# Kernel tuning notes

Hardware: AMD Instinct MI355X
Metric: run time of the kernel (lower is better)

## Reference

```python
import jax, jax.numpy as jnp
import numpy as np

K = 32
BN_EPS = 1e-5


def setup_inputs() -> dict:
    key = jax.random.key(0)
    ks = jax.random.split(key, 4)
    B, Cin, N, C = 8, 1152, 4096, 128
    return {
        "x": jax.random.normal(ks[0], (B, Cin, N), dtype=jnp.float32),
        "W1": jax.random.normal(ks[1], (C, Cin), dtype=jnp.float32) * 0.02,
        "bn_gamma": jnp.ones((C,), jnp.float32),
        "bn_beta": jnp.zeros((C,), jnp.float32),
        "bn_mean": jnp.zeros((C,), jnp.float32),
        "bn_var": jnp.ones((C,), jnp.float32),
        "Wq": jax.random.normal(ks[2], (C, C), dtype=jnp.float32) * 0.05,
        "Wk": jax.random.normal(ks[3], (C, C), dtype=jnp.float32) * 0.05,
    }


def _forward(x, W1, bn_gamma, bn_beta, bn_mean, bn_var, Wq, Wk):
    # conv1: 1x1 Conv1d (no bias) + BatchNorm (inference stats) + LeakyReLU(0.2)
    h = jnp.einsum('oc,bcn->bon', W1, x)                       # [B,128,N]
    h = (h - bn_mean[None, :, None]) * jax.lax.rsqrt(bn_var + BN_EPS)[None, :, None]
    h = h * bn_gamma[None, :, None] + bn_beta[None, :, None]
    h = jnp.where(h >= 0, h, 0.2 * h)
    f = jnp.transpose(h, (0, 2, 1))                            # [B,N,128]

    # ops.group: feature-space KNN + 'diff' grouping
    sq = jnp.sum(f * f, axis=-1)                               # [B,N]
    dist = sq[:, :, None] + sq[:, None, :] - 2.0 * jnp.einsum('bnc,bmc->bnm', f, f)
    _, idx = jax.lax.top_k(-dist, K)                           # [B,N,K]
    nb = jax.vmap(lambda fb, ib: fb[ib])(f, idx)               # [B,N,K,128]
    diff = nb - f[:, :, None, :]                               # neighbors - center

    # q/k 1x1 convs, per-point 1xK attention
    q = jnp.einsum('bnc,oc->bno', f, Wq)                       # [B,N,128]
    k = jnp.einsum('bnkc,oc->bnko', diff, Wk)                  # [B,N,K,128]
    energy = jnp.einsum('bnc,bnkc->bnk', q, k) / jnp.sqrt(jnp.float32(q.shape[-1]))
    attn = jax.nn.softmax(energy, axis=-1)                     # [B,N,K]

    # std over K (biased), then per-cloud standardize (unbiased std, torch default)
    s = jnp.std(attn, axis=-1)                                 # [B,N]
    mean = jnp.mean(s, axis=1, keepdims=True)
    std = jnp.std(s, axis=1, keepdims=True, ddof=1)
    z = (s - mean) / std
    return 1.0 / (1.0 + jnp.power(jnp.float32(20.0), -z))      # modified sigmoid


def reference(x, W1, bn_gamma, bn_beta, bn_mean, bn_var, Wq, Wk):
    return _forward(x, W1, bn_gamma, bn_beta, bn_mean, bn_var, Wq, Wk)
```

## Files before the change

### kernel.cpp

```cpp
#include <hip/hip_runtime.h>
#include <math.h>

#define B_   8
#define CIN  1152
#define NPTS 4096
#define CH   128
#define KNN  32

__global__ __launch_bounds__(256) void k_conv_bn(
    const float* __restrict__ x, const float* __restrict__ W1,
    const float* __restrict__ gamma, const float* __restrict__ beta,
    const float* __restrict__ bmean, const float* __restrict__ bvar,
    float* __restrict__ f)
{
  __shared__ float Wl[8][132];
  __shared__ float Xl[8][36];
  int bid = blockIdx.x;
  int b = bid & 7;
  int nbase = (bid >> 3) * 32;
  int t = threadIdx.x;
  int c0 = (t & 31) * 4, n0 = (t >> 5) * 4;
  double acc[4][4];
#pragma unroll
  for (int i = 0; i < 4; ++i)
#pragma unroll
    for (int j = 0; j < 4; ++j) acc[i][j] = 0.0;

  for (int k0 = 0; k0 < CIN; k0 += 8) {
    {
      int c = t >> 1, kp = (t & 1) * 4;
      float4 w4 = *(const float4*)&W1[(size_t)c * CIN + k0 + kp];
      Wl[kp + 0][c] = w4.x; Wl[kp + 1][c] = w4.y;
      Wl[kp + 2][c] = w4.z; Wl[kp + 3][c] = w4.w;
    }
    {
      int k = t >> 5, n = t & 31;
      Xl[k][n] = x[((size_t)b * CIN + (k0 + k)) * NPTS + nbase + n];
    }
    __syncthreads();
#pragma unroll
    for (int kk = 0; kk < 8; ++kk) {
      float4 a  = *(const float4*)&Wl[kk][c0];
      float4 b0 = *(const float4*)&Xl[kk][n0];
      double av[4] = {(double)a.x, (double)a.y, (double)a.z, (double)a.w};
      double bv[4] = {(double)b0.x, (double)b0.y, (double)b0.z, (double)b0.w};
#pragma unroll
      for (int i = 0; i < 4; ++i)
#pragma unroll
        for (int j = 0; j < 4; ++j) acc[i][j] = fma(av[i], bv[j], acc[i][j]);
    }
    __syncthreads();
  }
  double rs[4], gm[4], bt[4], mu[4];
#pragma unroll
  for (int i = 0; i < 4; ++i) {
    int c = c0 + i;
    rs[i] = 1.0 / sqrt((double)bvar[c] + 1e-5);
    gm[i] = (double)gamma[c]; bt[i] = (double)beta[c]; mu[i] = (double)bmean[c];
  }
#pragma unroll
  for (int j = 0; j < 4; ++j) {
    int n = nbase + n0 + j;
    float4 o;
    float* op = &o.x;
#pragma unroll
    for (int i = 0; i < 4; ++i) {
      double v = (acc[i][j] - mu[i]) * rs[i];
      v = v * gm[i] + bt[i];
      if (v < 0.0) v = 0.2 * v;
      op[i] = (float)v;
    }
    *(float4*)&f[((size_t)b * NPTS + n) * CH + c0] = o;
  }
}

__global__ __launch_bounds__(256) void k_sq(const float* __restrict__ f,
                                            double* __restrict__ sq)
{
  int row = blockIdx.x * 4 + (threadIdx.x >> 6);
  int lane = threadIdx.x & 63;
  float2 v = ((const float2*)f)[(size_t)row * 64 + lane];
  double s = (double)v.x * (double)v.x + (double)v.y * (double)v.y;
#pragma unroll
  for (int sft = 1; sft < 64; sft <<= 1) s += __shfl_xor(s, sft);
  if (lane == 0) sq[row] = s;
}

__global__ __launch_bounds__(256) void k_wqk(const float* __restrict__ Wq,
                                             const float* __restrict__ Wk,
                                             float* __restrict__ M)
{
  __shared__ float Ql[128][17];
  __shared__ float Kl[128][17];
  int t = threadIdx.x;
  int cb = blockIdx.x * 16;
  int db = blockIdx.y * 16;
  {
    int o = t >> 1, h = (t & 1) * 8;
    float4 a = *(const float4*)&Wq[(size_t)o * CH + cb + h];
    float4 b = *(const float4*)&Wq[(size_t)o * CH + cb + h + 4];
    Ql[o][h + 0] = a.x; Ql[o][h + 1] = a.y; Ql[o][h + 2] = a.z; Ql[o][h + 3] = a.w;
    Ql[o][h + 4] = b.x; Ql[o][h + 5] = b.y; Ql[o][h + 6] = b.z; Ql[o][h + 7] = b.w;
    float4 c4 = *(const float4*)&Wk[(size_t)o * CH + db + h];
    float4 d4 = *(const float4*)&Wk[(size_t)o * CH + db + h + 4];
    Kl[o][h + 0] = c4.x; Kl[o][h + 1] = c4.y; Kl[o][h + 2] = c4.z; Kl[o][h + 3] = c4.w;
    Kl[o][h + 4] = d4.x; Kl[o][h + 5] = d4.y; Kl[o][h + 6] = d4.z; Kl[o][h + 7] = d4.w;
  }
  __syncthreads();
  int ci = t >> 4, cj = t & 15;
  float acc = 0.f;
#pragma unroll 8
  for (int o = 0; o < 128; ++o) acc = fmaf(Ql[o][ci], Kl[o][cj], acc);
  M[(size_t)(cb + ci) * CH + db + cj] = acc;
}

__global__ __launch_bounds__(256) void k_qk(const float* __restrict__ f,
                                            const float* __restrict__ M,
                                            float* __restrict__ qk)
{
  __shared__ float Ft[128][68];
  __shared__ float Ml[128 * 128];
  int t = threadIdx.x;
  size_t rbase = (size_t)blockIdx.x * 64;
  {
    int r = t & 63, cp = (t >> 6) * 32;
    for (int i = 0; i < 8; ++i) {
      int c = cp + i * 4;
      float4 v = *(const float4*)&f[(rbase + r) * CH + c];
      Ft[c][r] = v.x; Ft[c + 1][r] = v.y; Ft[c + 2][r] = v.z; Ft[c + 3][r] = v.w;
    }
  }
  {
    const float4* Mg = (const float4*)M;
    float4* Md = (float4*)Ml;
    for (int i = 0; i < 16; ++i) Md[t + 256 * i] = Mg[t + 256 * i];
  }
  __syncthreads();
  int r0 = (t >> 4) * 4, c0 = (t & 15) * 8;
  float acc[4][8];
#pragma unroll
  for (int i = 0; i < 4; ++i)
#pragma unroll
    for (int j = 0; j < 8; ++j) acc[i][j] = 0.f;
#pragma unroll 8
  for (int k = 0; k < 128; ++k) {
    float4 a  = *(const float4*)&Ft[k][r0];
    float4 b0 = *(const float4*)&Ml[k * 128 + c0];
    float4 b1 = *(const float4*)&Ml[k * 128 + c0 + 4];
    float av[4] = {a.x, a.y, a.z, a.w};
    float bv[8] = {b0.x, b0.y, b0.z, b0.w, b1.x, b1.y, b1.z, b1.w};
#pragma unroll
    for (int i = 0; i < 4; ++i)
#pragma unroll
      for (int j = 0; j < 8; ++j) acc[i][j] = fmaf(av[i], bv[j], acc[i][j]);
  }
#pragma unroll
  for (int i = 0; i < 4; ++i) {
    float4 o0 = {acc[i][0], acc[i][1], acc[i][2], acc[i][3]};
    float4 o1 = {acc[i][4], acc[i][5], acc[i][6], acc[i][7]};
    *(float4*)&qk[(rbase + r0 + i) * CH + c0]     = o0;
    *(float4*)&qk[(rbase + r0 + i) * CH + c0 + 4] = o1;
  }
}

__global__ __launch_bounds__(256, 2) void k_dist(
    const float* __restrict__ f, const double* __restrict__ sq,
    float* __restrict__ D, int b, int rowoff)
{
  __shared__ float As[2][32][132];
  __shared__ float Bs[2][32][132];
  int t = threadIdx.x;
  int nb = rowoff + blockIdx.x * 128;
  int mb = blockIdx.y * 128;
  const float* fb = f + (size_t)b * NPTS * CH;

  int lr = t & 127;
  int cq = (t >> 7) * 16;

#pragma unroll
  for (int i = 0; i < 4; ++i) {
    int c = cq + i * 4;
    float4 v = *(const float4*)&fb[(size_t)(nb + lr) * CH + c];
    As[0][c + 0][lr] = v.x; As[0][c + 1][lr] = v.y;
    As[0][c + 2][lr] = v.z; As[0][c + 3][lr] = v.w;
    float4 u = *(const float4*)&fb[(size_t)(mb + lr) * CH + c];
    Bs[0][c + 0][lr] = u.x; Bs[0][c + 1][lr] = u.y;
    Bs[0][c + 2][lr] = u.z; Bs[0][c + 3][lr] = u.w;
  }
  __syncthreads();

  int r0 = (t >> 4) * 8, m0 = (t & 15) * 8;
  double acc[8][8];
#pragma unroll
  for (int i = 0; i < 8; ++i)
#pragma unroll
    for (int j = 0; j < 8; ++j) acc[i][j] = 0.0;

#pragma unroll
  for (int ch = 0; ch < 4; ++ch) {
    int p = ch & 1;
    float4 pa[4], pb[4];
    if (ch < 3) {
      int cbase = (ch + 1) * 32;
#pragma unroll
      for (int i = 0; i < 4; ++i) {
        pa[i] = *(const float4*)&fb[(size_t)(nb + lr) * CH + cbase + cq + i * 4];
        pb[i] = *(const float4*)&fb[(size_t)(mb + lr) * CH + cbase + cq + i * 4];
      }
    }
#pragma unroll 4
    for (int kk = 0; kk < 32; ++kk) {
      float4 a0 = *(const float4*)&As[p][kk][r0];
      float4 a1 = *(const float4*)&As[p][kk][r0 + 4];
      float4 b0 = *(const float4*)&Bs[p][kk][m0];
      float4 b1 = *(const float4*)&Bs[p][kk][m0 + 4];
      double av[8] = {(double)a0.x, (double)a0.y, (double)a0.z, (double)a0.w,
                      (double)a1.x, (double)a1.y, (double)a1.z, (double)a1.w};
      double bv[8] = {(double)b0.x, (double)b0.y, (double)b0.z, (double)b0.w,
                      (double)b1.x, (double)b1.y, (double)b1.z, (double)b1.w};
#pragma unroll
      for (int i = 0; i < 8; ++i)
#pragma unroll
        for (int j = 0; j < 8; ++j) acc[i][j] = fma(av[i], bv[j], acc[i][j]);
    }
    if (ch < 3) {
      int q = p ^ 1;
#pragma unroll
      for (int i = 0; i < 4; ++i) {
        int c = cq + i * 4;
        As[q][c + 0][lr] = pa[i].x; As[q][c + 1][lr] = pa[i].y;
        As[q][c + 2][lr] = pa[i].z; As[q][c + 3][lr] = pa[i].w;
        Bs[q][c + 0][lr] = pb[i].x; Bs[q][c + 1][lr] = pb[i].y;
        Bs[q][c + 2][lr] = pb[i].z; Bs[q][c + 3][lr] = pb[i].w;
      }
    }
    __syncthreads();
  }

  double sqn[8], sqm[8];
#pragma unroll
  for (int i = 0; i < 8; ++i) sqn[i] = sq[(size_t)b * NPTS + nb + r0 + i];
#pragma unroll
  for (int j = 0; j < 8; ++j) sqm[j] = sq[(size_t)b * NPTS + mb + m0 + j];
#pragma unroll
  for (int i = 0; i < 8; ++i) {
    int rloc = blockIdx.x * 128 + r0 + i;
    float4 o;
    o.x = (float)((sqn[i] + sqm[0]) - 2.0 * acc[i][0]);
    o.y = (float)((sqn[i] + sqm[1]) - 2.0 * acc[i][1]);
    o.z = (float)((sqn[i] + sqm[2]) - 2.0 * acc[i][2]);
    o.w = (float)((sqn[i] + sqm[3]) - 2.0 * acc[i][3]);
    *(float4*)&D[(size_t)rloc * NPTS + mb + m0] = o;
    o.x = (float)((sqn[i] + sqm[4]) - 2.0 * acc[i][4]);
    o.y = (float)((sqn[i] + sqm[5]) - 2.0 * acc[i][5]);
    o.z = (float)((sqn[i] + sqm[6]) - 2.0 * acc[i][6]);
    o.w = (float)((sqn[i] + sqm[7]) - 2.0 * acc[i][7]);
    *(float4*)&D[(size_t)rloc * NPTS + mb + m0 + 4] = o;
  }
}

__device__ __forceinline__ unsigned int sortkey(float x) {
  unsigned int u = __float_as_uint(x);
  return (u & 0x80000000u) ? ~u : (u | 0x80000000u);
}

__global__ __launch_bounds__(256) void k_select(
    const float* __restrict__ D, const float* __restrict__ f,
    const float* __restrict__ qk, float* __restrict__ sv,
    int b, int rowoff)
{
  __shared__ unsigned int keys[NPTS];
  __shared__ unsigned int hist[256];
  __shared__ unsigned int wsum[4];
  __shared__ unsigned int eqw[4];
  __shared__ unsigned int sh_bucket, sh_excl, nkept;
  __shared__ int   kept[KNN];
  __shared__ float qkl[CH];
  __shared__ float fc[CH];
  __shared__ float eng[KNN];

  int t = threadIdx.x;
  int row = rowoff + blockIdx.x;
  const float* fb = f + (size_t)b * NPTS * CH;

  {
    const float4* Dp = (const float4*)(D + (size_t)blockIdx.x * NPTS);
#pragma unroll
    for (int i = 0; i < 4; ++i) {
      float4 v = Dp[t + 256 * i];
      uint4 u;
      u.x = sortkey(v.x); u.y = sortkey(v.y);
      u.z = sortkey(v.z); u.w = sortkey(v.w);
      ((uint4*)keys)[t + 256 * i] = u;
    }
  }
  if (t == 0) nkept = 0;
  if (t < 32) {
    ((float4*)qkl)[t] = ((const float4*)(qk + ((size_t)b * NPTS + row) * CH))[t];
  } else if (t < 64) {
    ((float4*)fc)[t - 32] = ((const float4*)(fb + (size_t)row * CH))[t - 32];
  }
  __syncthreads();

  unsigned int prefix = 0;
  unsigned int target = KNN;
  unsigned int cnt_less = 0;
  for (int pass = 0; pass < 4; ++pass) {
    int shift = 24 - pass * 8;
    hist[t] = 0;
    __syncthreads();
#pragma unroll
    for (int i = 0; i < 16; ++i) {
      unsigned int k = keys[t + 256 * i];
      bool m = (pass == 0) || ((k >> (shift + 8)) == prefix);
      unsigned int bidx = (k >> shift) & 255u;
      bool pm = m;
#pragma unroll
      for (int it = 0; it < 4; ++it) {
        unsigned long long act = __ballot(pm);
        if (act == 0ull) break;
        int leader = (int)__ffsll((unsigned long long)act) - 1;
        unsigned int lb = __shfl(bidx, leader);
        bool same = pm && (bidx == lb);
        unsigned long long grp = __ballot(same);
        if ((t & 63) == leader)
          atomicAdd(&hist[lb], (unsigned int)__popcll(grp));
        pm = pm && !same;
      }
      if (pm) atomicAdd(&hist[bidx], 1u);
    }
    __syncthreads();
    unsigned int v = hist[t];
    unsigned int sc = v;
#pragma unroll
    for (int d = 1; d < 64; d <<= 1) {
      unsigned int nn = __shfl_up(sc, d);
      if ((t & 63) >= d) sc += nn;
    }
    if ((t & 63) == 63) wsum[t >> 6] = sc;
    __syncthreads();
    unsigned int wo = 0;
#pragma unroll
    for (int w = 0; w < 4; ++w) wo += (w < (t >> 6)) ? wsum[w] : 0u;
    unsigned int incl = sc + wo;
    unsigned int excl = incl - v;
    if (excl < target && target <= incl) { sh_bucket = (unsigned int)t; sh_excl = excl; }
    __syncthreads();
    prefix = (prefix << 8) | sh_bucket;
    target -= sh_excl;
    cnt_less += sh_excl;
    __syncthreads();
  }
  unsigned int thr_key = prefix;

#pragma unroll
  for (int i = 0; i < 16; ++i) {
    int idx = t + 256 * i;
    if (keys[idx] < thr_key) {
      unsigned int p = atomicAdd(&nkept, 1u);
      kept[p] = idx;
    }
  }
  {
    unsigned int eqloc = 0;
#pragma unroll
    for (int j = 0; j < 16; ++j)
      eqloc += (keys[t * 16 + ((j + t) & 15)] == thr_key) ? 1u : 0u;
    unsigned int esc = eqloc;
#pragma unroll
    for (int d = 1; d < 64; d <<= 1) {
      unsigned int nn = __shfl_up(esc, d);
      if ((t & 63) >= d) esc += nn;
    }
    if ((t & 63) == 63) eqw[t >> 6] = esc;
    __syncthreads();
    unsigned int ewo = 0;
#pragma unroll
    for (int w = 0; w < 4; ++w) ewo += (w < (t >> 6)) ? eqw[w] : 0u;
    unsigned int slot = cnt_less + (esc + ewo - eqloc);
#pragma unroll
    for (int j = 0; j < 16; ++j) {
      if (keys[t * 16 + j] == thr_key) {
        if (slot < KNN) kept[slot] = t * 16 + j;
        slot++;
      }
    }
  }
  __syncthreads();

  {
    int kk = t >> 3, lg = t & 7;
    int mg = kept[kk];
    const float* fm = fb + (size_t)mg * CH;
    float dd = 0.f, ds = 0.f;
#pragma unroll
    for (int i = 0; i < 4; ++i) {
      float4 qv = *(const float4*)&qkl[lg * 16 + i * 4];
      float4 vm = *(const float4*)&fm[lg * 16 + i * 4];
      float4 vc = *(const float4*)&fc[lg * 16 + i * 4];
      dd = fmaf(qv.x, vm.x, dd); dd = fmaf(qv.y, vm.y, dd);
      dd = fmaf(qv.z, vm.z, dd); dd = fmaf(qv.w, vm.w, dd);
      ds = fmaf(qv.x, vc.x, ds); ds = fmaf(qv.y, vc.y, ds);
      ds = fmaf(qv.z, vc.z, ds); ds = fmaf(qv.w, vc.w, ds);
    }
#pragma unroll
    for (int m = 1; m < 8; m <<= 1) { dd += __shfl_xor(dd, m); ds += __shfl_xor(ds, m); }
    if (lg == 0) eng[kk] = (dd - ds) * 0.08838834764831845f;
  }
  __syncthreads();

  if (t < 64) {
    float e = (t < 32) ? eng[t] : -INFINITY;
    float mx = e;
#pragma unroll
    for (int m = 1; m < 32; m <<= 1) mx = fmaxf(mx, __shfl_xor(mx, m));
    float ex = (t < 32) ? expf(e - mx) : 0.f;
    float sm = ex;
#pragma unroll
    for (int m = 1; m < 32; m <<= 1) sm += __shfl_xor(sm, m);
    float a  = (t < 32) ? (ex / sm) : 0.f;
    float sa = a;
#pragma unroll
    for (int m = 1; m < 32; m <<= 1) sa += __shfl_xor(sa, m);
    float mean = sa * (1.f / 32.f);
    float dv = (t < 32) ? (a - mean) : 0.f;
    float vr = dv * dv;
#pragma unroll
    for (int m = 1; m < 32; m <<= 1) vr += __shfl_xor(vr, m);
    if (t == 0) sv[(size_t)b * NPTS + row] = sqrtf(vr * (1.f / 32.f));
  }
}

__global__ __launch_bounds__(256) void k_final(const float* __restrict__ s,
                                               float* __restrict__ out)
{
  __shared__ float red[4];
  int b = blockIdx.x, t = threadIdx.x;
  const float4* sp = (const float4*)(s + (size_t)b * NPTS);
  float4* op = (float4*)(out + (size_t)b * NPTS);
  float4 vs[4];
  float loc = 0.f;
#pragma unroll
  for (int i = 0; i < 4; ++i) {
    vs[i] = sp[t + 256 * i];
    loc += vs[i].x + vs[i].y + vs[i].z + vs[i].w;
  }
#pragma unroll
  for (int sft = 1; sft < 64; sft <<= 1) loc += __shfl_xor(loc, sft);
  if ((t & 63) == 0) red[t >> 6] = loc;
  __syncthreads();
  float meanv = (red[0] + red[1] + red[2] + red[3]) * (1.f / 4096.f);
  __syncthreads();
  float loc2 = 0.f;
#pragma unroll
  for (int i = 0; i < 4; ++i) {
    float dx = vs[i].x - meanv, dy = vs[i].y - meanv;
    float dz = vs[i].z - meanv, dw = vs[i].w - meanv;
    loc2 += dx * dx + dy * dy + dz * dz + dw * dw;
  }
#pragma unroll
  for (int sft = 1; sft < 64; sft <<= 1) loc2 += __shfl_xor(loc2, sft);
  if ((t & 63) == 0) red[t >> 6] = loc2;
  __syncthreads();
  float var = (red[0] + red[1] + red[2] + red[3]) * (1.f / 4095.f);
  float rstd = rsqrtf(var);
  const float L20 = 4.3219280948873623f;
#pragma unroll
  for (int i = 0; i < 4; ++i) {
    float4 v = vs[i], o;
    o.x = 1.f / (1.f + exp2f(-(v.x - meanv) * rstd * L20));
    o.y = 1.f / (1.f + exp2f(-(v.y - meanv) * rstd * L20));
    o.z = 1.f / (1.f + exp2f(-(v.z - meanv) * rstd * L20));
    o.w = 1.f / (1.f + exp2f(-(v.w - meanv) * rstd * L20));
    op[t + 256 * i] = o;
  }
}

extern "C" void kernel_launch(void* const* d_in, const int* in_sizes, int n_in,
                              void* d_out, int out_size, void* d_ws, size_t ws_size,
                              hipStream_t stream)
{
  const float* x     = (const float*)d_in[0];
  const float* W1    = (const float*)d_in[1];
  const float* gamma = (const float*)d_in[2];
  const float* beta  = (const float*)d_in[3];
  const float* bmean = (const float*)d_in[4];
  const float* bvar  = (const float*)d_in[5];
  const float* Wq    = (const float*)d_in[6];
  const float* Wk    = (const float*)d_in[7];
  float* out = (float*)d_out;

  float*  f   = (float*)d_ws;
  float*  qk  = f  + (size_t)B_ * NPTS * CH;
  double* sqd = (double*)(qk + (size_t)B_ * NPTS * CH);
  float*  sv  = (float*)(sqd + (size_t)B_ * NPTS);
  float*  M   = sv + (size_t)B_ * NPTS;
  float*  D   = M  + (size_t)CH * CH;

  size_t fixed_bytes = (size_t)((char*)D - (char*)d_ws);
  size_t avail = (ws_size > fixed_bytes) ? (ws_size - fixed_bytes) : 0;
  int chunk = 1024;
  if (avail >= (size_t)4096 * NPTS * 4) chunk = 4096;
  else if (avail >= (size_t)2048 * NPTS * 4) chunk = 2048;

  hipLaunchKernelGGL(k_conv_bn, dim3(1024), dim3(256), 0, stream,
                     x, W1, gamma, beta, bmean, bvar, f);
  hipLaunchKernelGGL(k_sq, dim3(8192), dim3(256), 0, stream, f, sqd);
  hipLaunchKernelGGL(k_wqk, dim3(8, 8), dim3(256), 0, stream, Wq, Wk, M);
  hipLaunchKernelGGL(k_qk, dim3(512), dim3(256), 0, stream, f, M, qk);
  for (int b = 0; b < B_; ++b) {
    for (int ro = 0; ro < NPTS; ro += chunk) {
      hipLaunchKernelGGL(k_dist, dim3(chunk / 128, 32), dim3(256), 0, stream,
                         f, sqd, D, b, ro);
      hipLaunchKernelGGL(k_select, dim3(chunk), dim3(256), 0, stream,
                         D, f, qk, sv, b, ro);
    }
  }
  hipLaunchKernelGGL(k_final, dim3(8), dim3(256), 0, stream, sv, out);
}
```

Measured before the change: 1.920 ms.

## Exploit distance-matrix symmetry by computing only upper-triangular tiles

Adds a distance kernel that computes only the 528 lower-triangular 128x128 tiles of each batch's N×N distance matrix and writes each off-diagonal tile twice, once directly and once transposed through XOR-swizzled shared memory. It is used when the workspace can hold a full 4096-row chunk. The aim is to roughly halve the FP64 Gram-matrix FMA work that dominates the distance step. In exchange it adds a transpose pass through shared memory, extra syncs, and a triangular index decode, while the write traffic to D is unchanged.

```diff
diff --git a/kernel.cpp b/kernel.cpp
--- a/kernel.cpp
+++ b/kernel.cpp
@@ -163,6 +163,124 @@
   }
 }
 
+#define DTS 132
+__global__ __launch_bounds__(256, 2) void k_dist_sym(
+    const float* __restrict__ f, const double* __restrict__ sq,
+    float* __restrict__ D, int b)
+{
+  __shared__ float smem[16896];
+  float* As = smem;
+  float* Bs = smem + 2 * 32 * DTS;
+  int t = threadIdx.x;
+  int id = blockIdx.x;
+  int by = (int)((sqrtf(8.f * id + 1.f) - 1.f) * 0.5f);
+  while ((by + 1) * (by + 2) / 2 <= id) ++by;
+  while (by * (by + 1) / 2 > id) --by;
+  int bx = id - by * (by + 1) / 2;
+  int nb = bx * 128, mb = by * 128;
+  const float* fb = f + (size_t)b * NPTS * CH;
+
+  int lr = t & 127;
+  int cq = (t >> 7) * 16;
+
+#pragma unroll
+  for (int i = 0; i < 4; ++i) {
+    int c = cq + i * 4;
+    float4 v = *(const float4*)&fb[(size_t)(nb + lr) * CH + c];
+    As[(c + 0) * DTS + lr] = v.x; As[(c + 1) * DTS + lr] = v.y;
+    As[(c + 2) * DTS + lr] = v.z; As[(c + 3) * DTS + lr] = v.w;
+    float4 u = *(const float4*)&fb[(size_t)(mb + lr) * CH + c];
+    Bs[(c + 0) * DTS + lr] = u.x; Bs[(c + 1) * DTS + lr] = u.y;
+    Bs[(c + 2) * DTS + lr] = u.z; Bs[(c + 3) * DTS + lr] = u.w;
+  }
+  __syncthreads();
+
+  int r0 = (t >> 4) * 8, m0 = (t & 15) * 8;
+  double acc[8][8];
+#pragma unroll
+  for (int i = 0; i < 8; ++i)
+#pragma unroll
+    for (int j = 0; j < 8; ++j) acc[i][j] = 0.0;
+
+#pragma unroll
+  for (int ch = 0; ch < 4; ++ch) {
+    int p = ch & 1;
+    float4 pa[4], pb[4];
+    if (ch < 3) {
+      int cbase = (ch + 1) * 32;
+#pragma unroll
+      for (int i = 0; i < 4; ++i) {
+        pa[i] = *(const float4*)&fb[(size_t)(nb + lr) * CH + cbase + cq + i * 4];
+        pb[i] = *(const float4*)&fb[(size_t)(mb + lr) * CH + cbase + cq + i * 4];
+      }
+    }
+#pragma unroll 4
+    for (int kk = 0; kk < 32; ++kk) {
+      const float* Ap = &As[(p * 32 + kk) * DTS];
+      const float* Bp = &Bs[(p * 32 + kk) * DTS];
+      float4 a0 = *(const float4*)&Ap[r0];
+      float4 a1 = *(const float4*)&Ap[r0 + 4];
+      float4 b0 = *(const float4*)&Bp[m0];
+      float4 b1 = *(const float4*)&Bp[m0 + 4];
+      double av[8] = {(double)a0.x, (double)a0.y, (double)a0.z, (double)a0.w,
+                      (double)a1.x, (double)a1.y, (double)a1.z, (double)a1.w};
+      double bv[8] = {(double)b0.x, (double)b0.y, (double)b0.z, (double)b0.w,
+                      (double)b1.x, (double)b1.y, (double)b1.z, (double)b1.w};
+#pragma unroll
+      for (int i = 0; i < 8; ++i)
+#pragma unroll
+        for (int j = 0; j < 8; ++j) acc[i][j] = fma(av[i], bv[j], acc[i][j]);
+    }
+    if (ch < 3) {
+      int q = p ^ 1;
+#pragma unroll
+      for (int i = 0; i < 4; ++i) {
+        int c = cq + i * 4;
+        As[(q * 32 + c + 0) * DTS + lr] = pa[i].x; As[(q * 32 + c + 1) * DTS + lr] = pa[i].y;
+        As[(q * 32 + c + 2) * DTS + lr] = pa[i].z; As[(q * 32 + c + 3) * DTS + lr] = pa[i].w;
+        Bs[(q * 32 + c + 0) * DTS + lr] = pb[i].x; Bs[(q * 32 + c + 1) * DTS + lr] = pb[i].y;
+        Bs[(q * 32 + c + 2) * DTS + lr] = pb[i].z; Bs[(q * 32 + c + 3) * DTS + lr] = pb[i].w;
+      }
+    }
+    __syncthreads();
+  }
+
+  double sqn[8], sqm[8];
+#pragma unroll
+  for (int i = 0; i < 8; ++i) sqn[i] = sq[(size_t)b * NPTS + nb + r0 + i];
+#pragma unroll
+  for (int j = 0; j < 8; ++j) sqm[j] = sq[(size_t)b * NPTS + mb + m0 + j];
+
+  int xk = (t & 3) * 8;
+#pragma unroll
+  for (int i = 0; i < 8; ++i) {
+    float vr[8];
+#pragma unroll
+    for (int j = 0; j < 8; ++j) {
+      vr[j] = (float)((sqn[i] + sqm[j]) - 2.0 * acc[i][j]);
+      if (bx != by) smem[(m0 + j) * DTS + ((r0 + i) ^ xk)] = vr[j];
+    }
+    float4 o0 = {vr[0], vr[1], vr[2], vr[3]};
+    float4 o1 = {vr[4], vr[5], vr[6], vr[7]};
+    *(float4*)&D[(size_t)(nb + r0 + i) * NPTS + mb + m0]     = o0;
+    *(float4*)&D[(size_t)(nb + r0 + i) * NPTS + mb + m0 + 4] = o1;
+  }
+
+  if (bx != by) {
+    __syncthreads();
+#pragma unroll
+    for (int ph = 0; ph < 8; ++ph) {
+      int rr = ph * 16 + (t >> 4);
+      int cc = (t & 15) * 8;
+      int xr = ((rr >> 3) & 3) * 8;
+      float4 s0 = *(const float4*)&smem[rr * DTS + (cc ^ xr)];
+      float4 s1 = *(const float4*)&smem[rr * DTS + ((cc + 4) ^ xr)];
+      *(float4*)&D[(size_t)(mb + rr) * NPTS + nb + cc]     = s0;
+      *(float4*)&D[(size_t)(mb + rr) * NPTS + nb + cc + 4] = s1;
+    }
+  }
+}
+
 __global__ __launch_bounds__(256, 2) void k_dist(
     const float* __restrict__ f, const double* __restrict__ sq,
     float* __restrict__ D, int b, int rowoff)
@@ -508,12 +626,21 @@
   hipLaunchKernelGGL(k_sq, dim3(8192), dim3(256), 0, stream, f, sqd);
   hipLaunchKernelGGL(k_wqk, dim3(8, 8), dim3(256), 0, stream, Wq, Wk, M);
   hipLaunchKernelGGL(k_qk, dim3(512), dim3(256), 0, stream, f, M, qk);
-  for (int b = 0; b < B_; ++b) {
-    for (int ro = 0; ro < NPTS; ro += chunk) {
-      hipLaunchKernelGGL(k_dist, dim3(chunk / 128, 32), dim3(256), 0, stream,
-                         f, sqd, D, b, ro);
-      hipLaunchKernelGGL(k_select, dim3(chunk), dim3(256), 0, stream,
-                         D, f, qk, sv, b, ro);
+  if (chunk == 4096) {
+    for (int b = 0; b < B_; ++b) {
+      hipLaunchKernelGGL(k_dist_sym, dim3(528), dim3(256), 0, stream,
+                         f, sqd, D, b);
+      hipLaunchKernelGGL(k_select, dim3(4096), dim3(256), 0, stream,
+                         D, f, qk, sv, b, 0);
+    }
+  } else {
+    for (int b = 0; b < B_; ++b) {
+      for (int ro = 0; ro < NPTS; ro += chunk) {
+        hipLaunchKernelGGL(k_dist, dim3(chunk / 128, 32), dim3(256), 0, stream,
+                           f, sqd, D, b, ro);
+        hipLaunchKernelGGL(k_select, dim3(chunk), dim3(256), 0, stream,
+                           D, f, qk, sv, b, ro);
+      }
     }
   }
   hipLaunchKernelGGL(k_final, dim3(8), dim3(256), 0, stream, sv, out);
```

New measurement: 1.749 ms. 8.9% less time.
